# Performance work log

Measured on AMD Instinct MI355X. Metric: run time of the kernel, lower is better.

## Reference

```python
import jax, jax.numpy as jnp
import numpy as np

N_NODES = 50000
N_EDGES = 800000
IN_C, HID, OUT_C, T = 64, 64, 64, 16


def setup_inputs() -> dict:
    key = jax.random.key(0)
    ks = jax.random.split(key, 9)
    x = jax.random.normal(ks[0], (N_NODES, IN_C, T), dtype=jnp.float32)
    edge_index = jax.random.randint(ks[1], (2, N_EDGES), 0, N_NODES, dtype=jnp.int32)
    edge_attr = jax.random.uniform(ks[2], (N_EDGES, T), dtype=jnp.float32)
    s1 = 1.0 / np.sqrt(IN_C)
    s2 = 1.0 / np.sqrt(HID)
    s3 = 1.0 / np.sqrt(OUT_C)
    W1 = jax.random.uniform(ks[3], (IN_C, HID), jnp.float32, -s1, s1)
    b1 = jnp.zeros((HID,), jnp.float32)
    W2 = jax.random.uniform(ks[4], (HID, OUT_C), jnp.float32, -s2, s2)
    b2 = jnp.zeros((OUT_C,), jnp.float32)
    Wout = jax.random.uniform(ks[5], (OUT_C, OUT_C), jnp.float32, -s3, s3)
    bout = jax.random.uniform(ks[6], (OUT_C,), jnp.float32, -s3, s3)
    return {"x": x, "edge_index": edge_index, "edge_attr": edge_attr,
            "W1": W1, "b1": b1, "W2": W2, "b2": b2, "Wout": Wout, "bout": bout}


def _gcn_conv(h, src, dst, ew, W, b, n_nodes):
    # h: [N, d_in] -> [N, d_out]; GCNConv with edge weights + self-loops,
    # symmetric normalization D^-1/2 A D^-1/2, aggregation at dst (col).
    h = h @ W
    deg = jax.ops.segment_sum(ew, dst, num_segments=n_nodes) + 1.0  # self-loop weight 1
    dinv = jnp.where(deg > 0, deg ** -0.5, 0.0)
    norm = dinv[src] * ew * dinv[dst]                       # [E]
    agg = jax.ops.segment_sum(h[src] * norm[:, None], dst, num_segments=n_nodes)
    agg = agg + h * (dinv * dinv)[:, None]                  # self-loop message
    return agg + b


def reference(x, edge_index, edge_attr, W1, b1, W2, b2, Wout, bout):
    n_nodes = x.shape[0]
    xa = x.mean(axis=-1)                # temporal mean aggregation: [N, in_c]
    ew = edge_attr[:, -1]               # last-step edge weight: [E]
    src, dst = edge_index[0], edge_index[1]
    h = _gcn_conv(xa, src, dst, ew, W1, b1, n_nodes)
    h = jax.nn.relu(h)
    h = _gcn_conv(h, src, dst, ew, W2, b2, n_nodes)
    return h @ Wout + bout              # output head, Identity activation
```

## Files before the change

kernel.cpp:

```cpp
#include <hip/hip_runtime.h>

#define CAP 64
#define OVF_MAX 8192
#define WPAD 68


__global__ void k_pre(int* __restrict__ cur, int* __restrict__ ovfc, int N,
                      const float* __restrict__ W2, const float* __restrict__ Wout,
                      const float* __restrict__ b2, const float* __restrict__ bout,
                      float* __restrict__ WcT, float* __restrict__ bc, int zb) {
    int tid = threadIdx.x;
    int bid = blockIdx.x;
    if (bid < zb) {
        int n = bid * 256 + tid;
        if (n < N) cur[n] = 0;
        if (n == N) *ovfc = 0;
        return;
    }
    int wb = bid - zb;
    if (wb < 16) {
        int idx = wb * 256 + tid;
        int j = idx >> 6, i = idx & 63;
        float s = 0.0f;
        #pragma unroll 8
        for (int m = 0; m < 64; ++m)
            s = fmaf(W2[i * 64 + m], Wout[m * 64 + j], s);
        WcT[idx] = s;
    } else if (tid < 64) {
        float s = bout[tid];
        for (int k = 0; k < 64; ++k)
            s = fmaf(b2[k], Wout[k * 64 + tid], s);
        bc[tid] = s;
    }
}

__global__ __launch_bounds__(256) void k_scatmean(
        const int* __restrict__ ei, const float* __restrict__ ea,
        int* __restrict__ cur, int2* __restrict__ eb,
        int* __restrict__ ovf_cnt, int4* __restrict__ ovf,
        int E, int scatterBlocks,
        const float* __restrict__ x, const float* __restrict__ W1,
        float* __restrict__ h1, int N) {
    int tid = threadIdx.x;
    if ((int)blockIdx.x < scatterBlocks) {
        int e = blockIdx.x * 256 + tid;
        if (e < E) {
            int s = ei[e];
            int d = ei[E + e];
            float w = ea[(size_t)e * 16 + 15];
            int p = atomicAdd(cur + d, 1);
            if (p < CAP) {
                eb[(size_t)d * CAP + p] = make_int2(s, __float_as_int(w));
            } else {
                int q = atomicAdd(ovf_cnt, 1);
                if (q < OVF_MAX) ovf[q] = make_int4(s, d, __float_as_int(w), 0);
            }
        }
        return;
    }
    __shared__ float Wt[64 * WPAD];
    __shared__ float rbuf[4 * 64];
    {
        const float4* W4 = (const float4*)W1;
        #pragma unroll
        for (int i = 0; i < 4; ++i) {
            int f4 = i * 256 + tid;
            float4 v = W4[f4];
            int cc = f4 >> 4;
            int l0 = (f4 & 15) * 4;
            Wt[(l0 + 0) * WPAD + cc] = v.x;
            Wt[(l0 + 1) * WPAD + cc] = v.y;
            Wt[(l0 + 2) * WPAD + cc] = v.z;
            Wt[(l0 + 3) * WPAD + cc] = v.w;
        }
    }
    __syncthreads();
    int bid = (int)blockIdx.x - scatterBlocks;
    int w = tid >> 6, l = tid & 63;
    float* rw = rbuf + w * 64;
    for (int it = 0; it < 4; ++it) {
        int n = bid * 16 + it * 4 + w;
        if (n >= N) continue;
        const float4* xp = (const float4*)(x + (size_t)n * 1024);
        float4 v0 = xp[l], v1 = xp[64 + l], v2 = xp[128 + l], v3 = xp[192 + l];
        float s0 = (v0.x + v0.y) + (v0.z + v0.w);
        float s1 = (v1.x + v1.y) + (v1.z + v1.w);
        float s2 = (v2.x + v2.y) + (v2.z + v2.w);
        float s3 = (v3.x + v3.y) + (v3.z + v3.w);
        s0 += __shfl_xor(s0, 1); s0 += __shfl_xor(s0, 2);
        s1 += __shfl_xor(s1, 1); s1 += __shfl_xor(s1, 2);
        s2 += __shfl_xor(s2, 1); s2 += __shfl_xor(s2, 2);
        s3 += __shfl_xor(s3, 1); s3 += __shfl_xor(s3, 2);
        if ((l & 3) == 0) {
            int q = l >> 2;
            rw[q]      = s0 * 0.0625f;
            rw[q + 16] = s1 * 0.0625f;
            rw[q + 32] = s2 * 0.0625f;
            rw[q + 48] = s3 * 0.0625f;
        }
        float acc = 0.0f;
        const float4* rb4 = (const float4*)rw;
        const float4* wt4 = (const float4*)(Wt + l * WPAD);
        #pragma unroll
        for (int q = 0; q < 16; ++q) {
            float4 rv = rb4[q];
            float4 wv = wt4[q];
            acc = fmaf(rv.x, wv.x, acc);
            acc = fmaf(rv.y, wv.y, acc);
            acc = fmaf(rv.z, wv.z, acc);
            acc = fmaf(rv.w, wv.w, acc);
        }
        h1[(size_t)n * 64 + l] = acc;
    }
}

__global__ void k_dinvb(const int* __restrict__ cur, const int2* __restrict__ eb,
                        const int* __restrict__ ovf_cnt, const int4* __restrict__ ovf,
                        float* __restrict__ dinv, int N) {
    int tid = threadIdx.x;
    int n = blockIdx.x * 64 + (tid >> 2);
    int j = tid & 3;
    if (n >= N) return;
    int mfull = cur[n];
    int m = mfull > CAP ? CAP : mfull;
    float s = 0.0f;
    for (int i = j; i < m; i += 4) s += __int_as_float(eb[(size_t)n * CAP + i].y);
    s += __shfl_xor(s, 1);
    s += __shfl_xor(s, 2);
    if (j == 0) {
        if (mfull > CAP) {
            int oc = *ovf_cnt; if (oc > OVF_MAX) oc = OVF_MAX;
            for (int k = 0; k < oc; ++k) {
                int4 o = ovf[k];
                if (o.y == n) s += __int_as_float(o.z);
            }
        }
        dinv[n] = 1.0f / sqrtf(s + 1.0f);
    }
}

__global__ __launch_bounds__(256) void k_agg1(const float* __restrict__ in,
                                              const float* __restrict__ bias,
                                              const float* __restrict__ dinv,
                                              const int* __restrict__ cur,
                                              const int2* __restrict__ eb,
                                              const int* __restrict__ ovf_cnt,
                                              const int4* __restrict__ ovf,
                                              float* __restrict__ out, int N) {
    int tid = threadIdx.x;
    int w = tid >> 6, c = tid & 63;
    for (int it = 0; it < 4; ++it) {
        int n = blockIdx.x * 16 + it * 4 + w;
        if (n >= N) continue;
        float dv = dinv[n];
        float selfv = in[(size_t)n * 64 + c];
        float a0 = 0.f, a1 = 0.f, a2 = 0.f, a3 = 0.f;
        const int2* bkt = eb + (size_t)n * CAP;
        int mfull = cur[n];
        int m = mfull > CAP ? CAP : mfull;
        int i = 0;
        for (; i + 8 <= m; i += 8) {
            int2 e0 = bkt[i + 0], e1 = bkt[i + 1], e2 = bkt[i + 2], e3 = bkt[i + 3];
            int2 e4 = bkt[i + 4], e5 = bkt[i + 5], e6 = bkt[i + 6], e7 = bkt[i + 7];
            float d0 = dinv[e0.x], d1 = dinv[e1.x], d2 = dinv[e2.x], d3 = dinv[e3.x];
            float d4 = dinv[e4.x], d5 = dinv[e5.x], d6 = dinv[e6.x], d7 = dinv[e7.x];
            float v0 = in[(size_t)e0.x * 64 + c], v1 = in[(size_t)e1.x * 64 + c];
            float v2 = in[(size_t)e2.x * 64 + c], v3 = in[(size_t)e3.x * 64 + c];
            float v4 = in[(size_t)e4.x * 64 + c], v5 = in[(size_t)e5.x * 64 + c];
            float v6 = in[(size_t)e6.x * 64 + c], v7 = in[(size_t)e7.x * 64 + c];
            a0 = fmaf(v0, __int_as_float(e0.y) * d0, a0);
            a1 = fmaf(v1, __int_as_float(e1.y) * d1, a1);
            a2 = fmaf(v2, __int_as_float(e2.y) * d2, a2);
            a3 = fmaf(v3, __int_as_float(e3.y) * d3, a3);
            a0 = fmaf(v4, __int_as_float(e4.y) * d4, a0);
            a1 = fmaf(v5, __int_as_float(e5.y) * d5, a1);
            a2 = fmaf(v6, __int_as_float(e6.y) * d6, a2);
            a3 = fmaf(v7, __int_as_float(e7.y) * d7, a3);
        }
        for (; i < m; ++i) {
            int2 e = bkt[i];
            a0 = fmaf(in[(size_t)e.x * 64 + c], __int_as_float(e.y) * dinv[e.x], a0);
        }
        if (mfull > CAP) {
            int oc = *ovf_cnt; if (oc > OVF_MAX) oc = OVF_MAX;
            for (int k = 0; k < oc; ++k) {
                int4 o = ovf[k];
                if (o.y == n)
                    a0 = fmaf(in[(size_t)o.x * 64 + c], __int_as_float(o.z) * dinv[o.x], a0);
            }
        }
        float r = fmaf(dv, ((a0 + a1) + (a2 + a3)) + selfv * dv, bias[c]);
        out[(size_t)n * 64 + c] = fmaxf(r, 0.0f);
    }
}

__global__ __launch_bounds__(256) void k_agg2(const float* __restrict__ in,
                                              const float* __restrict__ WcT,
                                              const float* __restrict__ bc,
                                              const float* __restrict__ dinv,
                                              const int* __restrict__ cur,
                                              const int2* __restrict__ eb,
                                              const int* __restrict__ ovf_cnt,
                                              const int4* __restrict__ ovf,
                                              float* __restrict__ out, int N) {
    __shared__ float Wt[64 * WPAD];
    __shared__ float rbuf[4 * 64];
    int tid = threadIdx.x;
    {
        const float4* W4 = (const float4*)WcT;
        #pragma unroll
        for (int i = 0; i < 4; ++i) {
            int f4 = i * 256 + tid;
            float4 v = W4[f4];
            int j = f4 >> 4;
            int i0 = (f4 & 15) * 4;
            float4* dst = (float4*)(Wt + j * WPAD + i0);
            *dst = v;
        }
    }
    __syncthreads();
    int w = tid >> 6, c = tid & 63;
    float* rw = rbuf + w * 64;
    for (int it = 0; it < 4; ++it) {
        int n = blockIdx.x * 16 + it * 4 + w;
        if (n >= N) continue;
        float dv = dinv[n];
        float selfv = in[(size_t)n * 64 + c];
        float a0 = 0.f, a1 = 0.f, a2 = 0.f, a3 = 0.f;
        const int2* bkt = eb + (size_t)n * CAP;
        int mfull = cur[n];
        int m = mfull > CAP ? CAP : mfull;
        int i = 0;
        for (; i + 8 <= m; i += 8) {
            int2 e0 = bkt[i + 0], e1 = bkt[i + 1], e2 = bkt[i + 2], e3 = bkt[i + 3];
            int2 e4 = bkt[i + 4], e5 = bkt[i + 5], e6 = bkt[i + 6], e7 = bkt[i + 7];
            float d0 = dinv[e0.x], d1 = dinv[e1.x], d2 = dinv[e2.x], d3 = dinv[e3.x];
            float d4 = dinv[e4.x], d5 = dinv[e5.x], d6 = dinv[e6.x], d7 = dinv[e7.x];
            float v0 = in[(size_t)e0.x * 64 + c], v1 = in[(size_t)e1.x * 64 + c];
            float v2 = in[(size_t)e2.x * 64 + c], v3 = in[(size_t)e3.x * 64 + c];
            float v4 = in[(size_t)e4.x * 64 + c], v5 = in[(size_t)e5.x * 64 + c];
            float v6 = in[(size_t)e6.x * 64 + c], v7 = in[(size_t)e7.x * 64 + c];
            a0 = fmaf(v0, __int_as_float(e0.y) * d0, a0);
            a1 = fmaf(v1, __int_as_float(e1.y) * d1, a1);
            a2 = fmaf(v2, __int_as_float(e2.y) * d2, a2);
            a3 = fmaf(v3, __int_as_float(e3.y) * d3, a3);
            a0 = fmaf(v4, __int_as_float(e4.y) * d4, a0);
            a1 = fmaf(v5, __int_as_float(e5.y) * d5, a1);
            a2 = fmaf(v6, __int_as_float(e6.y) * d6, a2);
            a3 = fmaf(v7, __int_as_float(e7.y) * d7, a3);
        }
        for (; i < m; ++i) {
            int2 e = bkt[i];
            a0 = fmaf(in[(size_t)e.x * 64 + c], __int_as_float(e.y) * dinv[e.x], a0);
        }
        if (mfull > CAP) {
            int oc = *ovf_cnt; if (oc > OVF_MAX) oc = OVF_MAX;
            for (int k = 0; k < oc; ++k) {
                int4 o = ovf[k];
                if (o.y == n)
                    a0 = fmaf(in[(size_t)o.x * 64 + c], __int_as_float(o.z) * dinv[o.x], a0);
            }
        }
        float r = fmaf(dv, ((a0 + a1) + (a2 + a3)) + selfv * dv, 0.0f);
        rw[c] = r;
        float acc = bc[c];
        const float4* rb4 = (const float4*)rw;
        const float4* wt4 = (const float4*)(Wt + c * WPAD);
        #pragma unroll
        for (int q = 0; q < 16; ++q) {
            float4 rv = rb4[q];
            float4 wv = wt4[q];
            acc = fmaf(rv.x, wv.x, acc);
            acc = fmaf(rv.y, wv.y, acc);
            acc = fmaf(rv.z, wv.z, acc);
            acc = fmaf(rv.w, wv.w, acc);
        }
        out[(size_t)n * 64 + c] = acc;
    }
}


extern "C" void kernel_launch(void* const* d_in, const int* in_sizes, int n_in,
                              void* d_out, int out_size, void* d_ws, size_t ws_size,
                              hipStream_t stream) {
    const float* x    = (const float*)d_in[0];
    const int*   ei   = (const int*)d_in[1];
    const float* ea   = (const float*)d_in[2];
    const float* W1   = (const float*)d_in[3];
    const float* b1   = (const float*)d_in[4];
    const float* W2   = (const float*)d_in[5];
    const float* b2   = (const float*)d_in[6];
    const float* Wout = (const float*)d_in[7];
    const float* bout = (const float*)d_in[8];
    float* out = (float*)d_out;

    const int N = in_sizes[0] / (64 * 16);
    const int E = in_sizes[1] / 2;

    char* wsb = (char*)d_ws;
    int4*  ovf  = (int4*)wsb;
    int2*  eb   = (int2*)(wsb + OVF_MAX * 16);
    float* H1   = (float*)(wsb + OVF_MAX * 16 + (size_t)N * CAP * 8);
    size_t NC = (size_t)N * 64;
    float* Z    = H1 + NC;
    int*   cur  = (int*)(Z + NC);
    float* dinv = (float*)(cur + N);
    int*   ovfc = (int*)(dinv + N);
    float* WcT  = (float*)(ovfc + 4);
    float* bc   = WcT + 4096;

    dim3 b256(256);
    int meanBlocks    = (N + 15) / 16;
    int scatterBlocks = (E + 255) / 256;
    int zb = (N + 256) / 256;

    hipLaunchKernelGGL(k_pre, dim3(zb + 17), b256, 0, stream,
                       cur, ovfc, N, W2, Wout, b2, bout, WcT, bc, zb);
    hipLaunchKernelGGL(k_scatmean, dim3(scatterBlocks + meanBlocks), b256, 0, stream,
                       ei, ea, cur, eb, ovfc, ovf, E, scatterBlocks, x, W1, H1, N);
    hipLaunchKernelGGL(k_dinvb, dim3((N + 63) / 64), b256, 0, stream,
                       cur, eb, ovfc, ovf, dinv, N);
    hipLaunchKernelGGL(k_agg1, dim3(meanBlocks), b256, 0, stream,
                       H1, b1, dinv, cur, eb, ovfc, ovf, Z, N);
    hipLaunchKernelGGL(k_agg2, dim3(meanBlocks), b256, 0, stream,
                       Z, WcT, bc, dinv, cur, eb, ovfc, ovf, out, N);
}
```

Before: 202.6 us.

## Pad per-node atomic counters and batch four-node matvec with interleaved weight layout

Per-node bucket counters are spaced 16 ints apart so each scatter atomic lands on its own 64-byte region, which reduces same-line contention across destinations. The dense 64x64 matvecs in the mean and second-aggregation kernels are deferred until all four nodes per wave have been reduced. Each weight float4 loaded from LDS is then reused across four node rows, using a new interleaved shared-memory layout. The costs are a 16x larger counter array to zero and read with a strided pattern, plus more LDS per block.

```diff
diff --git a/kernel.cpp b/kernel.cpp
--- a/kernel.cpp
+++ b/kernel.cpp
@@ -2,19 +2,37 @@
 
 #define CAP 64
 #define OVF_MAX 8192
-#define WPAD 68
+#define CSTRIDE 16
+
+
+__device__ __forceinline__ void stage_Wt2(const float* __restrict__ W,
+                                          float* __restrict__ Wt2dw, int tid) {
+    const float4* W4 = (const float4*)W;
+    #pragma unroll
+    for (int i4 = 0; i4 < 4; ++i4) {
+        int f4 = i4 * 256 + tid;
+        float4 v = W4[f4];
+        int i  = f4 >> 4;
+        int c4 = f4 & 15;
+        int base = (i >> 2) * 256 + (i & 3);
+        Wt2dw[base + (4 * c4 + 0) * 4] = v.x;
+        Wt2dw[base + (4 * c4 + 1) * 4] = v.y;
+        Wt2dw[base + (4 * c4 + 2) * 4] = v.z;
+        Wt2dw[base + (4 * c4 + 3) * 4] = v.w;
+    }
+}
 
 
 __global__ void k_pre(int* __restrict__ cur, int* __restrict__ ovfc, int N,
                       const float* __restrict__ W2, const float* __restrict__ Wout,
                       const float* __restrict__ b2, const float* __restrict__ bout,
-                      float* __restrict__ WcT, float* __restrict__ bc, int zb) {
+                      float* __restrict__ Wc, float* __restrict__ bc, int zb) {
     int tid = threadIdx.x;
     int bid = blockIdx.x;
     if (bid < zb) {
-        int n = bid * 256 + tid;
-        if (n < N) cur[n] = 0;
-        if (n == N) *ovfc = 0;
+        int i = bid * 256 + tid;
+        if (i < N * CSTRIDE) cur[i] = 0;
+        if (i == N * CSTRIDE) *ovfc = 0;
         return;
     }
     int wb = bid - zb;
@@ -25,7 +43,7 @@
         #pragma unroll 8
         for (int m = 0; m < 64; ++m)
             s = fmaf(W2[i * 64 + m], Wout[m * 64 + j], s);
-        WcT[idx] = s;
+        Wc[i * 64 + j] = s;
     } else if (tid < 64) {
         float s = bout[tid];
         for (int k = 0; k < 64; ++k)
@@ -48,7 +66,7 @@
             int s = ei[e];
             int d = ei[E + e];
             float w = ea[(size_t)e * 16 + 15];
-            int p = atomicAdd(cur + d, 1);
+            int p = atomicAdd(cur + (size_t)d * CSTRIDE, 1);
             if (p < CAP) {
                 eb[(size_t)d * CAP + p] = make_int2(s, __float_as_int(w));
             } else {
@@ -58,28 +76,17 @@
         }
         return;
     }
-    __shared__ float Wt[64 * WPAD];
-    __shared__ float rbuf[4 * 64];
-    {
-        const float4* W4 = (const float4*)W1;
-        #pragma unroll
-        for (int i = 0; i < 4; ++i) {
-            int f4 = i * 256 + tid;
-            float4 v = W4[f4];
-            int cc = f4 >> 4;
-            int l0 = (f4 & 15) * 4;
-            Wt[(l0 + 0) * WPAD + cc] = v.x;
-            Wt[(l0 + 1) * WPAD + cc] = v.y;
-            Wt[(l0 + 2) * WPAD + cc] = v.z;
-            Wt[(l0 + 3) * WPAD + cc] = v.w;
-        }
-    }
+    __shared__ float Wt2[4096];
+    __shared__ float rbuf[4 * 4 * 64];
+    stage_Wt2(W1, Wt2, tid);
     __syncthreads();
     int bid = (int)blockIdx.x - scatterBlocks;
     int w = tid >> 6, l = tid & 63;
-    float* rw = rbuf + w * 64;
+    float* rw = rbuf + w * 256;
+    int n0 = bid * 16 + w;
+    #pragma unroll
     for (int it = 0; it < 4; ++it) {
-        int n = bid * 16 + it * 4 + w;
+        int n = n0 + it * 4;
         if (n >= N) continue;
         const float4* xp = (const float4*)(x + (size_t)n * 1024);
         float4 v0 = xp[l], v1 = xp[64 + l], v2 = xp[128 + l], v3 = xp[192 + l];
@@ -93,25 +100,36 @@
         s3 += __shfl_xor(s3, 1); s3 += __shfl_xor(s3, 2);
         if ((l & 3) == 0) {
             int q = l >> 2;
-            rw[q]      = s0 * 0.0625f;
-            rw[q + 16] = s1 * 0.0625f;
-            rw[q + 32] = s2 * 0.0625f;
-            rw[q + 48] = s3 * 0.0625f;
-        }
-        float acc = 0.0f;
-        const float4* rb4 = (const float4*)rw;
-        const float4* wt4 = (const float4*)(Wt + l * WPAD);
-        #pragma unroll
-        for (int q = 0; q < 16; ++q) {
-            float4 rv = rb4[q];
-            float4 wv = wt4[q];
-            acc = fmaf(rv.x, wv.x, acc);
-            acc = fmaf(rv.y, wv.y, acc);
-            acc = fmaf(rv.z, wv.z, acc);
-            acc = fmaf(rv.w, wv.w, acc);
-        }
-        h1[(size_t)n * 64 + l] = acc;
-    }
+            float* r = rw + it * 64;
+            r[q]      = s0 * 0.0625f;
+            r[q + 16] = s1 * 0.0625f;
+            r[q + 32] = s2 * 0.0625f;
+            r[q + 48] = s3 * 0.0625f;
+        }
+    }
+    float acc0 = 0.f, acc1 = 0.f, acc2 = 0.f, acc3 = 0.f;
+    const float4* wt4 = (const float4*)Wt2;
+    const float4* rb0 = (const float4*)(rw);
+    const float4* rb1 = (const float4*)(rw + 64);
+    const float4* rb2 = (const float4*)(rw + 128);
+    const float4* rb3 = (const float4*)(rw + 192);
+    #pragma unroll
+    for (int q = 0; q < 16; ++q) {
+        float4 wv = wt4[q * 64 + l];
+        float4 r0 = rb0[q], r1 = rb1[q], r2 = rb2[q], r3 = rb3[q];
+        acc0 = fmaf(r0.x, wv.x, acc0); acc0 = fmaf(r0.y, wv.y, acc0);
+        acc0 = fmaf(r0.z, wv.z, acc0); acc0 = fmaf(r0.w, wv.w, acc0);
+        acc1 = fmaf(r1.x, wv.x, acc1); acc1 = fmaf(r1.y, wv.y, acc1);
+        acc1 = fmaf(r1.z, wv.z, acc1); acc1 = fmaf(r1.w, wv.w, acc1);
+        acc2 = fmaf(r2.x, wv.x, acc2); acc2 = fmaf(r2.y, wv.y, acc2);
+        acc2 = fmaf(r2.z, wv.z, acc2); acc2 = fmaf(r2.w, wv.w, acc2);
+        acc3 = fmaf(r3.x, wv.x, acc3); acc3 = fmaf(r3.y, wv.y, acc3);
+        acc3 = fmaf(r3.z, wv.z, acc3); acc3 = fmaf(r3.w, wv.w, acc3);
+    }
+    if (n0 < N)      h1[(size_t)(n0     ) * 64 + l] = acc0;
+    if (n0 + 4 < N)  h1[(size_t)(n0 + 4 ) * 64 + l] = acc1;
+    if (n0 + 8 < N)  h1[(size_t)(n0 + 8 ) * 64 + l] = acc2;
+    if (n0 + 12 < N) h1[(size_t)(n0 + 12) * 64 + l] = acc3;
 }
 
 __global__ void k_dinvb(const int* __restrict__ cur, const int2* __restrict__ eb,
@@ -121,7 +139,7 @@
     int n = blockIdx.x * 64 + (tid >> 2);
     int j = tid & 3;
     if (n >= N) return;
-    int mfull = cur[n];
+    int mfull = cur[(size_t)n * CSTRIDE];
     int m = mfull > CAP ? CAP : mfull;
     float s = 0.0f;
     for (int i = j; i < m; i += 4) s += __int_as_float(eb[(size_t)n * CAP + i].y);
@@ -149,6 +167,7 @@
                                               float* __restrict__ out, int N) {
     int tid = threadIdx.x;
     int w = tid >> 6, c = tid & 63;
+    float bias_c = bias[c];
     for (int it = 0; it < 4; ++it) {
         int n = blockIdx.x * 16 + it * 4 + w;
         if (n >= N) continue;
@@ -156,7 +175,7 @@
         float selfv = in[(size_t)n * 64 + c];
         float a0 = 0.f, a1 = 0.f, a2 = 0.f, a3 = 0.f;
         const int2* bkt = eb + (size_t)n * CAP;
-        int mfull = cur[n];
+        int mfull = cur[(size_t)n * CSTRIDE];
         int m = mfull > CAP ? CAP : mfull;
         int i = 0;
         for (; i + 8 <= m; i += 8) {
@@ -189,13 +208,13 @@
                     a0 = fmaf(in[(size_t)o.x * 64 + c], __int_as_float(o.z) * dinv[o.x], a0);
             }
         }
-        float r = fmaf(dv, ((a0 + a1) + (a2 + a3)) + selfv * dv, bias[c]);
+        float r = fmaf(dv, ((a0 + a1) + (a2 + a3)) + selfv * dv, bias_c);
         out[(size_t)n * 64 + c] = fmaxf(r, 0.0f);
     }
 }
 
 __global__ __launch_bounds__(256) void k_agg2(const float* __restrict__ in,
-                                              const float* __restrict__ WcT,
+                                              const float* __restrict__ Wc,
                                               const float* __restrict__ bc,
                                               const float* __restrict__ dinv,
                                               const int* __restrict__ cur,
@@ -203,32 +222,24 @@
                                               const int* __restrict__ ovf_cnt,
                                               const int4* __restrict__ ovf,
                                               float* __restrict__ out, int N) {
-    __shared__ float Wt[64 * WPAD];
-    __shared__ float rbuf[4 * 64];
-    int tid = threadIdx.x;
-    {
-        const float4* W4 = (const float4*)WcT;
-        #pragma unroll
-        for (int i = 0; i < 4; ++i) {
-            int f4 = i * 256 + tid;
-            float4 v = W4[f4];
-            int j = f4 >> 4;
-            int i0 = (f4 & 15) * 4;
-            float4* dst = (float4*)(Wt + j * WPAD + i0);
-            *dst = v;
-        }
-    }
+    __shared__ float Wt2[4096];
+    __shared__ float rbuf[4 * 4 * 64];
+    int tid = threadIdx.x;
+    stage_Wt2(Wc, Wt2, tid);
     __syncthreads();
     int w = tid >> 6, c = tid & 63;
-    float* rw = rbuf + w * 64;
+    float bc_c = bc[c];
+    float* rw = rbuf + w * 256;
+    int n0 = blockIdx.x * 16 + w;
+    #pragma unroll
     for (int it = 0; it < 4; ++it) {
-        int n = blockIdx.x * 16 + it * 4 + w;
+        int n = n0 + it * 4;
         if (n >= N) continue;
         float dv = dinv[n];
         float selfv = in[(size_t)n * 64 + c];
         float a0 = 0.f, a1 = 0.f, a2 = 0.f, a3 = 0.f;
         const int2* bkt = eb + (size_t)n * CAP;
-        int mfull = cur[n];
+        int mfull = cur[(size_t)n * CSTRIDE];
         int m = mfull > CAP ? CAP : mfull;
         int i = 0;
         for (; i + 8 <= m; i += 8) {
@@ -261,22 +272,31 @@
                     a0 = fmaf(in[(size_t)o.x * 64 + c], __int_as_float(o.z) * dinv[o.x], a0);
             }
         }
-        float r = fmaf(dv, ((a0 + a1) + (a2 + a3)) + selfv * dv, 0.0f);
-        rw[c] = r;
-        float acc = bc[c];
-        const float4* rb4 = (const float4*)rw;
-        const float4* wt4 = (const float4*)(Wt + c * WPAD);
-        #pragma unroll
-        for (int q = 0; q < 16; ++q) {
-            float4 rv = rb4[q];
-            float4 wv = wt4[q];
-            acc = fmaf(rv.x, wv.x, acc);
-            acc = fmaf(rv.y, wv.y, acc);
-            acc = fmaf(rv.z, wv.z, acc);
-            acc = fmaf(rv.w, wv.w, acc);
-        }
-        out[(size_t)n * 64 + c] = acc;
-    }
+        rw[it * 64 + c] = dv * (((a0 + a1) + (a2 + a3)) + selfv * dv);
+    }
+    float acc0 = bc_c, acc1 = bc_c, acc2 = bc_c, acc3 = bc_c;
+    const float4* wt4 = (const float4*)Wt2;
+    const float4* rb0 = (const float4*)(rw);
+    const float4* rb1 = (const float4*)(rw + 64);
+    const float4* rb2 = (const float4*)(rw + 128);
+    const float4* rb3 = (const float4*)(rw + 192);
+    #pragma unroll
+    for (int q = 0; q < 16; ++q) {
+        float4 wv = wt4[q * 64 + c];
+        float4 r0 = rb0[q], r1 = rb1[q], r2 = rb2[q], r3 = rb3[q];
+        acc0 = fmaf(r0.x, wv.x, acc0); acc0 = fmaf(r0.y, wv.y, acc0);
+        acc0 = fmaf(r0.z, wv.z, acc0); acc0 = fmaf(r0.w, wv.w, acc0);
+        acc1 = fmaf(r1.x, wv.x, acc1); acc1 = fmaf(r1.y, wv.y, acc1);
+        acc1 = fmaf(r1.z, wv.z, acc1); acc1 = fmaf(r1.w, wv.w, acc1);
+        acc2 = fmaf(r2.x, wv.x, acc2); acc2 = fmaf(r2.y, wv.y, acc2);
+        acc2 = fmaf(r2.z, wv.z, acc2); acc2 = fmaf(r2.w, wv.w, acc2);
+        acc3 = fmaf(r3.x, wv.x, acc3); acc3 = fmaf(r3.y, wv.y, acc3);
+        acc3 = fmaf(r3.z, wv.z, acc3); acc3 = fmaf(r3.w, wv.w, acc3);
+    }
+    if (n0 < N)      out[(size_t)(n0     ) * 64 + c] = acc0;
+    if (n0 + 4 < N)  out[(size_t)(n0 + 4 ) * 64 + c] = acc1;
+    if (n0 + 8 < N)  out[(size_t)(n0 + 8 ) * 64 + c] = acc2;
+    if (n0 + 12 < N) out[(size_t)(n0 + 12) * 64 + c] = acc3;
 }
 
 
@@ -304,18 +324,18 @@
     size_t NC = (size_t)N * 64;
     float* Z    = H1 + NC;
     int*   cur  = (int*)(Z + NC);
-    float* dinv = (float*)(cur + N);
+    float* dinv = (float*)(cur + (size_t)N * CSTRIDE);
     int*   ovfc = (int*)(dinv + N);
-    float* WcT  = (float*)(ovfc + 4);
-    float* bc   = WcT + 4096;
+    float* Wc   = (float*)(ovfc + 4);
+    float* bc   = Wc + 4096;
 
     dim3 b256(256);
     int meanBlocks    = (N + 15) / 16;
     int scatterBlocks = (E + 255) / 256;
-    int zb = (N + 256) / 256;
+    int zb = (N * CSTRIDE + 256) / 256;
 
     hipLaunchKernelGGL(k_pre, dim3(zb + 17), b256, 0, stream,
-                       cur, ovfc, N, W2, Wout, b2, bout, WcT, bc, zb);
+                       cur, ovfc, N, W2, Wout, b2, bout, Wc, bc, zb);
     hipLaunchKernelGGL(k_scatmean, dim3(scatterBlocks + meanBlocks), b256, 0, stream,
                        ei, ea, cur, eb, ovfc, ovf, E, scatterBlocks, x, W1, H1, N);
     hipLaunchKernelGGL(k_dinvb, dim3((N + 63) / 64), b256, 0, stream,
@@ -323,5 +343,5 @@
     hipLaunchKernelGGL(k_agg1, dim3(meanBlocks), b256, 0, stream,
                        H1, b1, dinv, cur, eb, ovfc, ovf, Z, N);
     hipLaunchKernelGGL(k_agg2, dim3(meanBlocks), b256, 0, stream,
-                       Z, WcT, bc, dinv, cur, eb, ovfc, ovf, out, N);
-}
+                       Z, Wc, bc, dinv, cur, eb, ovfc, ovf, out, N);
+}
```

Measured after the change: 363.1 us. 1.79x slower.
